# Kernel tuning notes

Hardware: AMD Instinct MI355X
Metric: run time of the kernel (lower is better)

Reference implementation:

```python
import jax, jax.numpy as jnp
import numpy as np
import jax.lax as lax

B, S, E, H = 8, 4096, 1024, 128
TAU = 1.0
MIN_K = 32

def setup_inputs() -> dict:
    key = jax.random.key(0)
    k0, k1, k2, k3 = jax.random.split(key, 4)
    token_embeddings = jax.random.normal(k0, (B, S, E), dtype=jnp.float32)
    w1 = jax.random.normal(k1, (E, H), dtype=jnp.float32) * (1.0 / np.sqrt(E))
    b1 = jnp.zeros((H,), dtype=jnp.float32)
    w2 = jax.random.normal(k2, (H, 1), dtype=jnp.float32) * (1.0 / np.sqrt(H))
    b2 = jnp.zeros((1,), dtype=jnp.float32)
    # uniform noise for Gumbel, same bounds as the original module
    u = jax.random.uniform(k3, (B, S), minval=1e-08, maxval=1.0 - 1e-08, dtype=jnp.float32)
    return {"token_embeddings": token_embeddings, "w1": w1, "b1": b1, "w2": w2, "b2": b2, "u": u}

def reference(token_embeddings, w1, b1, w2, b2, u):
    # scorer MLP: Dense(H) -> relu -> Dense(1), squeeze -> [B, S]
    h = jax.nn.relu(jnp.einsum('bse,eh->bsh', token_embeddings, w1) + b1)
    importance_logits = (jnp.einsum('bsh,ho->bso', h, w2) + b2)[..., 0]  # [B, S]

    # expected_k (value_function is None): soft count of kept tokens
    expected_k = jax.nn.sigmoid(importance_logits).sum(axis=-1)  # [B]
    k = jnp.clip(expected_k.astype(jnp.int32), MIN_K, None)      # [B]

    # Gumbel-softmax top-k, hard=True
    gumbel = -jnp.log(-jnp.log(u))
    soft_mask = jax.nn.softmax((importance_logits + gumbel) / TAU, axis=-1)  # [B, S]

    # hard mask: 1.0 at the top-k[i] positions of soft_mask per row.
    # Equivalent to the original argsort + while_loop scatter: positions with
    # descending-sort rank < k[i] get 1.0.
    order = jnp.argsort(-soft_mask, axis=-1)          # [B, S] descending order
    ranks = jnp.argsort(order, axis=-1)               # rank of each position
    hard_mask = (ranks < k[:, None]).astype(soft_mask.dtype)

    selection_mask = lax.stop_gradient(hard_mask - soft_mask) + soft_mask
    filtered_embeddings = token_embeddings * selection_mask[..., None]
    return filtered_embeddings, selection_mask, expected_k
```

## Files before the change

### kernel.cpp

```cpp
#include <hip/hip_runtime.h>
#include <hip/hip_bf16.h>
#include <math.h>

#define B_ 8
#define S_ 4096
#define E_ 1024
#define H_ 128
#define MIN_K 32
#define OUT_MASK_OFF (B_*S_*E_)
#define OUT_EK_OFF   (B_*S_*E_ + B_*S_)

#define Z_OFF      0
#define SOFT_OFF   131072
#define CNT_OFF    262144
#define KROW_OFF   393216
#define PARTS_OFF  393248
#define PARTM_OFF  397344
#define W1T_HI_OFF 399392
#define W1T_LO_OFF 661536

typedef __attribute__((ext_vector_type(8))) short   frag8;
typedef __attribute__((ext_vector_type(4))) float   fragc;
typedef __attribute__((ext_vector_type(4))) unsigned short us4;

static __device__ __forceinline__ unsigned short bf16_rne(float f) {
  unsigned u = __float_as_uint(f);
  unsigned r = u + 0x7FFF + ((u >> 16) & 1);
  return (unsigned short)(r >> 16);
}
static __device__ __forceinline__ float bf16_to_f32(unsigned short h) {
  return __uint_as_float(((unsigned)h) << 16);
}

__global__ __launch_bounds__(256) void prep_w_kernel(
    const float* __restrict__ w1,
    unsigned short* __restrict__ w1t_hi, unsigned short* __restrict__ w1t_lo)
{
  int id = blockIdx.x * 256 + threadIdx.x;
  int k  = id >> 5;
  int n4 = id & 31;
  float4 w = *(const float4*)(w1 + k * H_ + n4 * 4);
#pragma unroll
  for (int e = 0; e < 4; ++e) {
    float f = (e == 0) ? w.x : (e == 1) ? w.y : (e == 2) ? w.z : w.w;
    unsigned short hi = bf16_rne(f);
    unsigned short lo = bf16_rne(f - bf16_to_f32(hi));
    int n = n4 * 4 + e;
    w1t_hi[n * E_ + k] = hi;
    w1t_lo[n * E_ + k] = lo;
  }
}

#define KT 32
#define LDST 40

__global__ __launch_bounds__(256) void scorer_kernel(
    const float* __restrict__ x,
    const unsigned short* __restrict__ w1t_hi,
    const unsigned short* __restrict__ w1t_lo,
    const float* __restrict__ b1, const float* __restrict__ w2,
    const float* __restrict__ b2, const float* __restrict__ u,
    float* __restrict__ zout, double* __restrict__ partS,
    float* __restrict__ partM)
{
  __shared__ unsigned short xs_hi[128 * LDST];
  __shared__ unsigned short xs_lo[128 * LDST];
  __shared__ unsigned short bs_hi[128 * LDST];
  __shared__ unsigned short bs_lo[128 * LDST];
  __shared__ float part[4][64];

  const int tid  = threadIdx.x;
  const int wave = tid >> 6;
  const int lane = tid & 63;
  const int l15  = lane & 15;
  const int quad = lane >> 4;
  const int wr   = wave >> 1;
  const int wc   = wave & 1;
  const int m0   = blockIdx.x * 128;

  fragc acc[4][4];
#pragma unroll
  for (int i = 0; i < 4; ++i)
#pragma unroll
    for (int j = 0; j < 4; ++j) acc[i][j] = (fragc)(0.f);

  int sm[4], skq[4];
#pragma unroll
  for (int i = 0; i < 4; ++i) { int idx = tid + i * 256; sm[i] = idx >> 3; skq[i] = idx & 7; }
  int bn[2], bkq[2];
#pragma unroll
  for (int i = 0; i < 2; ++i) { int idx = tid + i * 256; bn[i] = idx >> 2; bkq[i] = idx & 3; }

  float4 p[4];
  uint4  qh[2], ql[2];
#pragma unroll
  for (int i = 0; i < 4; ++i)
    p[i] = *(const float4*)(x + (size_t)(m0 + sm[i]) * E_ + skq[i] * 4);
#pragma unroll
  for (int i = 0; i < 2; ++i) {
    size_t off = (size_t)bn[i] * E_ + bkq[i] * 8;
    qh[i] = *(const uint4*)(w1t_hi + off);
    ql[i] = *(const uint4*)(w1t_lo + off);
  }

  for (int k0 = 0; k0 < E_; k0 += KT) {
    __syncthreads();
#pragma unroll
    for (int i = 0; i < 4; ++i) {
      us4 h4, l4;
      float fv[4] = {p[i].x, p[i].y, p[i].z, p[i].w};
#pragma unroll
      for (int e = 0; e < 4; ++e) {
        unsigned short hi = bf16_rne(fv[e]);
        h4[e] = hi; l4[e] = bf16_rne(fv[e] - bf16_to_f32(hi));
      }
      *(us4*)&xs_hi[sm[i] * LDST + skq[i] * 4] = h4;
      *(us4*)&xs_lo[sm[i] * LDST + skq[i] * 4] = l4;
    }
#pragma unroll
    for (int i = 0; i < 2; ++i) {
      *(uint4*)&bs_hi[bn[i] * LDST + bkq[i] * 8] = qh[i];
      *(uint4*)&bs_lo[bn[i] * LDST + bkq[i] * 8] = ql[i];
    }
    __syncthreads();

    if (k0 + KT < E_) {
#pragma unroll
      for (int i = 0; i < 4; ++i)
        p[i] = *(const float4*)(x + (size_t)(m0 + sm[i]) * E_ + (k0 + KT) + skq[i] * 4);
#pragma unroll
      for (int i = 0; i < 2; ++i) {
        size_t off = (size_t)bn[i] * E_ + (k0 + KT) + bkq[i] * 8;
        qh[i] = *(const uint4*)(w1t_hi + off);
        ql[i] = *(const uint4*)(w1t_lo + off);
      }
    }

    frag8 bh[4], bl[4];
#pragma unroll
    for (int ntl = 0; ntl < 4; ++ntl) {
      int a = ((wc * 4 + ntl) * 16 + l15) * LDST + quad * 8;
      bh[ntl] = *(const frag8*)&bs_hi[a];
      bl[ntl] = *(const frag8*)&bs_lo[a];
    }
#pragma unroll
    for (int mtl = 0; mtl < 4; ++mtl) {
      int a = ((wr * 4 + mtl) * 16 + l15) * LDST + quad * 8;
      frag8 ah = *(const frag8*)&xs_hi[a];
      frag8 al = *(const frag8*)&xs_lo[a];
#pragma unroll
      for (int ntl = 0; ntl < 4; ++ntl) {
        acc[mtl][ntl] = __builtin_amdgcn_mfma_f32_16x16x32_bf16(ah, bh[ntl], acc[mtl][ntl], 0, 0, 0);
        acc[mtl][ntl] = __builtin_amdgcn_mfma_f32_16x16x32_bf16(ah, bl[ntl], acc[mtl][ntl], 0, 0, 0);
        acc[mtl][ntl] = __builtin_amdgcn_mfma_f32_16x16x32_bf16(al, bh[ntl], acc[mtl][ntl], 0, 0, 0);
      }
    }
  }

  float b1v[4], w2v[4];
#pragma unroll
  for (int ntl = 0; ntl < 4; ++ntl) {
    int n = (wc * 4 + ntl) * 16 + l15;
    b1v[ntl] = b1[n]; w2v[ntl] = w2[n];
  }
  float v[4][4];
#pragma unroll
  for (int mtl = 0; mtl < 4; ++mtl)
#pragma unroll
    for (int reg = 0; reg < 4; ++reg) {
      float pv = 0.f;
#pragma unroll
      for (int ntl = 0; ntl < 4; ++ntl) {
        float h = acc[mtl][ntl][reg] + b1v[ntl];
        h = h > 0.f ? h : 0.f;
        pv = fmaf(h, w2v[ntl], pv);
      }
      v[mtl][reg] = pv;
    }
#pragma unroll
  for (int mask = 1; mask < 16; mask <<= 1)
#pragma unroll
    for (int mtl = 0; mtl < 4; ++mtl)
#pragma unroll
      for (int reg = 0; reg < 4; ++reg)
        v[mtl][reg] += __shfl_xor(v[mtl][reg], mask);

  if (l15 == 0) {
#pragma unroll
    for (int mtl = 0; mtl < 4; ++mtl)
#pragma unroll
      for (int reg = 0; reg < 4; ++reg)
        part[wave][mtl * 16 + quad * 4 + reg] = v[mtl][reg];
  }
  __syncthreads();

  if (tid < 128) {
    const int wgrp = tid >> 6;
    const int token = m0 + tid;
    float L = part[wgrp * 2][tid & 63] + part[wgrp * 2 + 1][tid & 63] + b2[0];
    float g = -logf(-logf(u[token]));
    float z = L + g;
    zout[token] = z;
    double s = (double)(1.f / (1.f + expf(-L)));
    float zm = z;
#pragma unroll
    for (int mask = 1; mask < 64; mask <<= 1) {
      s += __shfl_xor(s, mask);
      zm = fmaxf(zm, __shfl_xor(zm, mask));
    }
    if ((tid & 63) == 0) {
      int pidx = blockIdx.x * 2 + wgrp;
      partS[pidx] = s;
      partM[pidx] = zm;
    }
  }
}

__global__ __launch_bounds__(1024) void softmax_kernel(
    const float* __restrict__ z, const double* __restrict__ partS,
    const float* __restrict__ partM, float* __restrict__ soft,
    int* __restrict__ krow, float* __restrict__ ek_out)
{
  const int b = blockIdx.x;
  const int t = threadIdx.x;
  __shared__ float m_sh;
  __shared__ double ek_sh;
  __shared__ double wp[16];
  __shared__ float den_sh;

  if (t < 64) {
    double ps = partS[b * 64 + t];
    float  pm = partM[b * 64 + t];
#pragma unroll
    for (int mask = 1; mask < 64; mask <<= 1) {
      ps += __shfl_xor(ps, mask);
      pm = fmaxf(pm, __shfl_xor(pm, mask));
    }
    if (t == 0) { ek_sh = ps; m_sh = pm; }
  }
  __syncthreads();
  float m = m_sh;

  float e[4];
  double pe = 0.0;
#pragma unroll
  for (int i = 0; i < 4; ++i) {
    e[i] = expf(z[b * S_ + t + i * 1024] - m);
    pe += (double)e[i];
  }
#pragma unroll
  for (int mask = 1; mask < 64; mask <<= 1) pe += __shfl_xor(pe, mask);
  if ((t & 63) == 0) wp[t >> 6] = pe;
  __syncthreads();
  if (t < 16) {
    double vv = wp[t];
#pragma unroll
    for (int mask = 1; mask < 16; mask <<= 1) vv += __shfl_xor(vv, mask);
    if (t == 0) den_sh = (float)vv;
  }
  __syncthreads();
  float den = den_sh;
#pragma unroll
  for (int i = 0; i < 4; ++i) soft[b * S_ + t + i * 1024] = e[i] / den;

  if (t == 0) {
    float ekf = (float)ek_sh;
    int k = (int)ekf;
    if (k < MIN_K) k = MIN_K;
    krow[b] = k;
    ek_out[b] = ekf;
  }
}

__global__ __launch_bounds__(256) void rank_kernel(
    const float* __restrict__ soft, int* __restrict__ counts)
{
  __shared__ float4 sjs[256];
  const int b  = blockIdx.z;
  const int ic = blockIdx.x;
  const int jc = blockIdx.y;
  const int tid = threadIdx.x;
  const float* row = soft + b * S_;

  sjs[tid] = ((const float4*)row)[jc * 256 + tid];
  const int i = ic * 256 + tid;
  const float si = row[i];
  __syncthreads();

  int cnt = 0;
  const int jbase = jc * 1024;
  for (int j4 = 0; j4 < 256; ++j4) {
    float4 vv = sjs[j4];
    int j = jbase + j4 * 4;
    cnt += (vv.x > si) || (vv.x == si && (j + 0) < i);
    cnt += (vv.y > si) || (vv.y == si && (j + 1) < i);
    cnt += (vv.z > si) || (vv.z == si && (j + 2) < i);
    cnt += (vv.w > si) || (vv.w == si && (j + 3) < i);
  }
  atomicAdd(&counts[b * S_ + i], cnt);
}

__global__ __launch_bounds__(256) void filter_kernel(
    const float* __restrict__ x, const float* __restrict__ soft,
    const int* __restrict__ counts, const int* __restrict__ krow,
    float* __restrict__ out, float* __restrict__ mask_out)
{
  const int token = blockIdx.x;
  const int b = token >> 12;
  const float s = soft[token];
  const float h = (counts[token] < krow[b]) ? 1.f : 0.f;
  const float sel = (h - s) + s;

  size_t base = (size_t)token * (E_ / 4) + threadIdx.x;
  if (sel == 0.f) {
    ((float4*)out)[base] = make_float4(0.f, 0.f, 0.f, 0.f);
  } else {
    float4 v = ((const float4*)x)[base];
    v.x *= sel; v.y *= sel; v.z *= sel; v.w *= sel;
    ((float4*)out)[base] = v;
  }
  if (threadIdx.x == 0) mask_out[token] = sel;
}

extern "C" void kernel_launch(void* const* d_in, const int* in_sizes, int n_in,
                              void* d_out, int out_size, void* d_ws, size_t ws_size,
                              hipStream_t stream) {
  const float* x  = (const float*)d_in[0];
  const float* w1 = (const float*)d_in[1];
  const float* b1 = (const float*)d_in[2];
  const float* w2 = (const float*)d_in[3];
  const float* b2 = (const float*)d_in[4];
  const float* u  = (const float*)d_in[5];

  float* out = (float*)d_out;
  float* out_filt = out;
  float* out_mask = out + OUT_MASK_OFF;
  float* out_ek   = out + OUT_EK_OFF;

  char* ws = (char*)d_ws;
  float*          ws_z      = (float*)(ws + Z_OFF);
  float*          ws_soft   = (float*)(ws + SOFT_OFF);
  int*            ws_cnt    = (int*)(ws + CNT_OFF);
  int*            ws_krow   = (int*)(ws + KROW_OFF);
  double*         ws_partS  = (double*)(ws + PARTS_OFF);
  float*          ws_partM  = (float*)(ws + PARTM_OFF);
  unsigned short* ws_w1thi  = (unsigned short*)(ws + W1T_HI_OFF);
  unsigned short* ws_w1tlo  = (unsigned short*)(ws + W1T_LO_OFF);

  hipMemsetAsync(ws_cnt, 0, B_ * S_ * sizeof(int), stream);
  prep_w_kernel<<<dim3(128), dim3(256), 0, stream>>>(w1, ws_w1thi, ws_w1tlo);
  scorer_kernel<<<dim3(B_ * S_ / 128), dim3(256), 0, stream>>>(
      x, ws_w1thi, ws_w1tlo, b1, w2, b2, u, ws_z, ws_partS, ws_partM);
  softmax_kernel<<<dim3(B_), dim3(1024), 0, stream>>>(
      ws_z, ws_partS, ws_partM, ws_soft, ws_krow, out_ek);
  rank_kernel<<<dim3(16, 4, 8), dim3(256), 0, stream>>>(ws_soft, ws_cnt);
  filter_kernel<<<dim3(B_ * S_), dim3(256), 0, stream>>>(
      x, ws_soft, ws_cnt, ws_krow, out_filt, out_mask);
}
```

Before: 346.4 us.

## Shrink scorer tile to 32 tokens and read W1 fragments directly from global

The scorer GEMM goes from 128-token tiles with both operands staged in LDS to 32-token tiles. Each wave now owns 32 of the 128 hidden columns and loads its W1 hi/lo bf16 fragments straight from global memory (L2-resident), with the K step doubled to 64. This quadruples the grid (1024 blocks) to fill more CUs and cuts LDS use, at the cost of more redundant W1 traffic per token. The softmax kernel's partial-reduction layout and the workspace offsets are updated to match the 128 partials per row.

```diff
diff --git a/kernel.cpp b/kernel.cpp
--- a/kernel.cpp
+++ b/kernel.cpp
@@ -15,9 +15,9 @@
 #define CNT_OFF    262144
 #define KROW_OFF   393216
 #define PARTS_OFF  393248
-#define PARTM_OFF  397344
-#define W1T_HI_OFF 399392
-#define W1T_LO_OFF 661536
+#define PARTM_OFF  401440
+#define W1T_HI_OFF 405536
+#define W1T_LO_OFF 667680
 
 typedef __attribute__((ext_vector_type(8))) short   frag8;
 typedef __attribute__((ext_vector_type(4))) float   fragc;
@@ -51,8 +51,8 @@
   }
 }
 
-#define KT 32
-#define LDST 40
+#define KT 64
+#define LDST 72
 
 __global__ __launch_bounds__(256) void scorer_kernel(
     const float* __restrict__ x,
@@ -63,50 +63,36 @@
     float* __restrict__ zout, double* __restrict__ partS,
     float* __restrict__ partM)
 {
-  __shared__ unsigned short xs_hi[128 * LDST];
-  __shared__ unsigned short xs_lo[128 * LDST];
-  __shared__ unsigned short bs_hi[128 * LDST];
-  __shared__ unsigned short bs_lo[128 * LDST];
-  __shared__ float part[4][64];
+  __shared__ unsigned short xs_hi[32 * LDST];
+  __shared__ unsigned short xs_lo[32 * LDST];
+  __shared__ float part[4][32];
 
   const int tid  = threadIdx.x;
   const int wave = tid >> 6;
   const int lane = tid & 63;
   const int l15  = lane & 15;
   const int quad = lane >> 4;
-  const int wr   = wave >> 1;
-  const int wc   = wave & 1;
-  const int m0   = blockIdx.x * 128;
-
-  fragc acc[4][4];
-#pragma unroll
-  for (int i = 0; i < 4; ++i)
-#pragma unroll
-    for (int j = 0; j < 4; ++j) acc[i][j] = (fragc)(0.f);
-
-  int sm[4], skq[4];
-#pragma unroll
-  for (int i = 0; i < 4; ++i) { int idx = tid + i * 256; sm[i] = idx >> 3; skq[i] = idx & 7; }
-  int bn[2], bkq[2];
-#pragma unroll
-  for (int i = 0; i < 2; ++i) { int idx = tid + i * 256; bn[i] = idx >> 2; bkq[i] = idx & 3; }
-
-  float4 p[4];
-  uint4  qh[2], ql[2];
-#pragma unroll
-  for (int i = 0; i < 4; ++i)
+  const int m0   = blockIdx.x * 32;
+
+  fragc acc[2][2];
+#pragma unroll
+  for (int i = 0; i < 2; ++i)
+#pragma unroll
+    for (int j = 0; j < 2; ++j) acc[i][j] = (fragc)(0.f);
+
+  int sm[2], skq[2];
+#pragma unroll
+  for (int i = 0; i < 2; ++i) { int idx = tid + i * 256; sm[i] = idx >> 4; skq[i] = idx & 15; }
+
+  float4 p[2];
+#pragma unroll
+  for (int i = 0; i < 2; ++i)
     p[i] = *(const float4*)(x + (size_t)(m0 + sm[i]) * E_ + skq[i] * 4);
-#pragma unroll
-  for (int i = 0; i < 2; ++i) {
-    size_t off = (size_t)bn[i] * E_ + bkq[i] * 8;
-    qh[i] = *(const uint4*)(w1t_hi + off);
-    ql[i] = *(const uint4*)(w1t_lo + off);
-  }
 
   for (int k0 = 0; k0 < E_; k0 += KT) {
     __syncthreads();
 #pragma unroll
-    for (int i = 0; i < 4; ++i) {
+    for (int i = 0; i < 2; ++i) {
       us4 h4, l4;
       float fv[4] = {p[i].x, p[i].y, p[i].z, p[i].w};
 #pragma unroll
@@ -117,101 +103,92 @@
       *(us4*)&xs_hi[sm[i] * LDST + skq[i] * 4] = h4;
       *(us4*)&xs_lo[sm[i] * LDST + skq[i] * 4] = l4;
     }
-#pragma unroll
-    for (int i = 0; i < 2; ++i) {
-      *(uint4*)&bs_hi[bn[i] * LDST + bkq[i] * 8] = qh[i];
-      *(uint4*)&bs_lo[bn[i] * LDST + bkq[i] * 8] = ql[i];
-    }
     __syncthreads();
 
     if (k0 + KT < E_) {
 #pragma unroll
-      for (int i = 0; i < 4; ++i)
+      for (int i = 0; i < 2; ++i)
         p[i] = *(const float4*)(x + (size_t)(m0 + sm[i]) * E_ + (k0 + KT) + skq[i] * 4);
-#pragma unroll
-      for (int i = 0; i < 2; ++i) {
-        size_t off = (size_t)bn[i] * E_ + (k0 + KT) + bkq[i] * 8;
-        qh[i] = *(const uint4*)(w1t_hi + off);
-        ql[i] = *(const uint4*)(w1t_lo + off);
+    }
+
+#pragma unroll
+    for (int ks = 0; ks < 2; ++ks) {
+      frag8 ah[2], al[2];
+#pragma unroll
+      for (int mt = 0; mt < 2; ++mt) {
+        int a = (mt * 16 + l15) * LDST + ks * 32 + quad * 8;
+        ah[mt] = *(const frag8*)&xs_hi[a];
+        al[mt] = *(const frag8*)&xs_lo[a];
       }
-    }
-
-    frag8 bh[4], bl[4];
-#pragma unroll
-    for (int ntl = 0; ntl < 4; ++ntl) {
-      int a = ((wc * 4 + ntl) * 16 + l15) * LDST + quad * 8;
-      bh[ntl] = *(const frag8*)&bs_hi[a];
-      bl[ntl] = *(const frag8*)&bs_lo[a];
-    }
-#pragma unroll
-    for (int mtl = 0; mtl < 4; ++mtl) {
-      int a = ((wr * 4 + mtl) * 16 + l15) * LDST + quad * 8;
-      frag8 ah = *(const frag8*)&xs_hi[a];
-      frag8 al = *(const frag8*)&xs_lo[a];
-#pragma unroll
-      for (int ntl = 0; ntl < 4; ++ntl) {
-        acc[mtl][ntl] = __builtin_amdgcn_mfma_f32_16x16x32_bf16(ah, bh[ntl], acc[mtl][ntl], 0, 0, 0);
-        acc[mtl][ntl] = __builtin_amdgcn_mfma_f32_16x16x32_bf16(ah, bl[ntl], acc[mtl][ntl], 0, 0, 0);
-        acc[mtl][ntl] = __builtin_amdgcn_mfma_f32_16x16x32_bf16(al, bh[ntl], acc[mtl][ntl], 0, 0, 0);
+#pragma unroll
+      for (int nt = 0; nt < 2; ++nt) {
+        int n = wave * 32 + nt * 16 + l15;
+        size_t off = (size_t)n * E_ + k0 + ks * 32 + quad * 8;
+        frag8 bh = *(const frag8*)(w1t_hi + off);
+        frag8 bl = *(const frag8*)(w1t_lo + off);
+#pragma unroll
+        for (int mt = 0; mt < 2; ++mt) {
+          acc[mt][nt] = __builtin_amdgcn_mfma_f32_16x16x32_bf16(ah[mt], bh, acc[mt][nt], 0, 0, 0);
+          acc[mt][nt] = __builtin_amdgcn_mfma_f32_16x16x32_bf16(ah[mt], bl, acc[mt][nt], 0, 0, 0);
+          acc[mt][nt] = __builtin_amdgcn_mfma_f32_16x16x32_bf16(al[mt], bh, acc[mt][nt], 0, 0, 0);
+        }
       }
     }
   }
 
-  float b1v[4], w2v[4];
-#pragma unroll
-  for (int ntl = 0; ntl < 4; ++ntl) {
-    int n = (wc * 4 + ntl) * 16 + l15;
-    b1v[ntl] = b1[n]; w2v[ntl] = w2[n];
-  }
-  float v[4][4];
-#pragma unroll
-  for (int mtl = 0; mtl < 4; ++mtl)
+  float b1v[2], w2v[2];
+#pragma unroll
+  for (int nt = 0; nt < 2; ++nt) {
+    int n = wave * 32 + nt * 16 + l15;
+    b1v[nt] = b1[n]; w2v[nt] = w2[n];
+  }
+  float v[2][4];
+#pragma unroll
+  for (int mt = 0; mt < 2; ++mt)
 #pragma unroll
     for (int reg = 0; reg < 4; ++reg) {
       float pv = 0.f;
 #pragma unroll
-      for (int ntl = 0; ntl < 4; ++ntl) {
-        float h = acc[mtl][ntl][reg] + b1v[ntl];
+      for (int nt = 0; nt < 2; ++nt) {
+        float h = acc[mt][nt][reg] + b1v[nt];
         h = h > 0.f ? h : 0.f;
-        pv = fmaf(h, w2v[ntl], pv);
+        pv = fmaf(h, w2v[nt], pv);
       }
-      v[mtl][reg] = pv;
+      v[mt][reg] = pv;
     }
 #pragma unroll
   for (int mask = 1; mask < 16; mask <<= 1)
 #pragma unroll
-    for (int mtl = 0; mtl < 4; ++mtl)
+    for (int mt = 0; mt < 2; ++mt)
 #pragma unroll
       for (int reg = 0; reg < 4; ++reg)
-        v[mtl][reg] += __shfl_xor(v[mtl][reg], mask);
+        v[mt][reg] += __shfl_xor(v[mt][reg], mask);
 
   if (l15 == 0) {
 #pragma unroll
-    for (int mtl = 0; mtl < 4; ++mtl)
+    for (int mt = 0; mt < 2; ++mt)
 #pragma unroll
       for (int reg = 0; reg < 4; ++reg)
-        part[wave][mtl * 16 + quad * 4 + reg] = v[mtl][reg];
-  }
-  __syncthreads();
-
-  if (tid < 128) {
-    const int wgrp = tid >> 6;
+        part[wave][mt * 16 + quad * 4 + reg] = v[mt][reg];
+  }
+  __syncthreads();
+
+  if (tid < 32) {
     const int token = m0 + tid;
-    float L = part[wgrp * 2][tid & 63] + part[wgrp * 2 + 1][tid & 63] + b2[0];
+    float L = ((part[0][tid] + part[1][tid]) + (part[2][tid] + part[3][tid])) + b2[0];
     float g = -logf(-logf(u[token]));
     float z = L + g;
     zout[token] = z;
     double s = (double)(1.f / (1.f + expf(-L)));
     float zm = z;
 #pragma unroll
-    for (int mask = 1; mask < 64; mask <<= 1) {
+    for (int mask = 1; mask < 32; mask <<= 1) {
       s += __shfl_xor(s, mask);
       zm = fmaxf(zm, __shfl_xor(zm, mask));
     }
-    if ((tid & 63) == 0) {
-      int pidx = blockIdx.x * 2 + wgrp;
-      partS[pidx] = s;
-      partM[pidx] = zm;
+    if (tid == 0) {
+      partS[blockIdx.x] = s;
+      partM[blockIdx.x] = zm;
     }
   }
 }
@@ -223,23 +200,23 @@
 {
   const int b = blockIdx.x;
   const int t = threadIdx.x;
-  __shared__ float m_sh;
-  __shared__ double ek_sh;
+  __shared__ double sS[2];
+  __shared__ float  sM[2];
   __shared__ double wp[16];
   __shared__ float den_sh;
 
-  if (t < 64) {
-    double ps = partS[b * 64 + t];
-    float  pm = partM[b * 64 + t];
+  if (t < 128) {
+    double ps = partS[b * 128 + t];
+    float  pm = partM[b * 128 + t];
 #pragma unroll
     for (int mask = 1; mask < 64; mask <<= 1) {
       ps += __shfl_xor(ps, mask);
       pm = fmaxf(pm, __shfl_xor(pm, mask));
     }
-    if (t == 0) { ek_sh = ps; m_sh = pm; }
-  }
-  __syncthreads();
-  float m = m_sh;
+    if ((t & 63) == 0) { sS[t >> 6] = ps; sM[t >> 6] = pm; }
+  }
+  __syncthreads();
+  const float m = fmaxf(sM[0], sM[1]);
 
   float e[4];
   double pe = 0.0;
@@ -264,7 +241,7 @@
   for (int i = 0; i < 4; ++i) soft[b * S_ + t + i * 1024] = e[i] / den;
 
   if (t == 0) {
-    float ekf = (float)ek_sh;
+    float ekf = (float)(sS[0] + sS[1]);
     int k = (int)ekf;
     if (k < MIN_K) k = MIN_K;
     krow[b] = k;
@@ -349,7 +326,7 @@
 
   hipMemsetAsync(ws_cnt, 0, B_ * S_ * sizeof(int), stream);
   prep_w_kernel<<<dim3(128), dim3(256), 0, stream>>>(w1, ws_w1thi, ws_w1tlo);
-  scorer_kernel<<<dim3(B_ * S_ / 128), dim3(256), 0, stream>>>(
+  scorer_kernel<<<dim3(B_ * S_ / 32), dim3(256), 0, stream>>>(
       x, ws_w1thi, ws_w1tlo, b1, w2, b2, u, ws_z, ws_partS, ws_partM);
   softmax_kernel<<<dim3(B_), dim3(1024), 0, stream>>>(
       ws_z, ws_partS, ws_partM, ws_soft, ws_krow, out_ek);
```

Measured after the change: 337.4 us. 1.03x faster.
